# Optimization experiments

Measured on AMD Instinct MI355X. Metric: run time of the kernel, lower is better.

## Reference

```python
import jax, jax.numpy as jnp
import numpy as np

GN_EPS = 1e-5
G = 8          # SKA groups
SKS3 = 27      # sks**3


def _aff(x, s, b):
    # folded BatchNorm (eval): per-channel scale + shift on NCDHW tensor
    return x * s[None, :, None, None, None] + b[None, :, None, None, None]


def _c1(x, w):
    # 1x1x1 conv as channel GEMM; w: [O, I]
    return jnp.einsum('bcdhw,oc->bodhw', x, w)


def _dw5(x, w):
    # depthwise 5x5x5 conv, pad=2; w: [C, 1, 5, 5, 5]
    return jax.lax.conv_general_dilated(
        x, w, window_strides=(1, 1, 1), padding=[(2, 2)] * 3,
        dimension_numbers=('NCDHW', 'OIDHW', 'NCDHW'),
        feature_group_count=x.shape[1])


def setup_inputs() -> dict:
    key = jax.random.key(0)
    ks = jax.random.split(key, 24)
    B, C, D, H, W = 2, 64, 32, 32, 32

    def n(k, shape, scale=1.0):
        return jax.random.normal(k, shape, jnp.float32) * scale

    def u(k, shape):
        return jax.random.uniform(k, shape, jnp.float32, 0.5, 1.5)

    return {
        'x': n(ks[0], (B, C, D, H, W)),
        'w1': n(ks[1], (32, 64), 64 ** -0.5),
        's1': u(ks[2], (32,)), 'b1': n(ks[3], (32,), 0.1),
        'w2': n(ks[4], (32, 1, 5, 5, 5), 125 ** -0.5),
        's2': u(ks[5], (32,)), 'b2': n(ks[6], (32,), 0.1),
        'w3': n(ks[7], (32, 32), 32 ** -0.5),
        's3': u(ks[8], (32,)), 'b3': n(ks[9], (32,), 0.1),
        'w4': n(ks[10], (216, 32), 32 ** -0.5), 'b4': n(ks[11], (216,), 0.1),
        'gn_g': u(ks[12], (216,)), 'gn_b': n(ks[13], (216,), 0.1),
        'bn_s': u(ks[14], (64,)), 'bn_b': n(ks[15], (64,), 0.1),
        'pw1_w': n(ks[16], (128, 64), 64 ** -0.5),
        'pw1_s': u(ks[17], (128,)), 'pw1_b': n(ks[18], (128,), 0.1),
        'pw2_w': n(ks[19], (64, 128), 128 ** -0.5),
        'pw2_s': u(ks[20], (64,)), 'pw2_b': n(ks[21], (64,), 0.1),
    }


def reference(x, w1, s1, b1, w2, s2, b2, w3, s3, b3, w4, b4,
              gn_g, gn_b, bn_s, bn_b,
              pw1_w, pw1_s, pw1_b, pw2_w, pw2_s, pw2_b):
    B, C, D, H, W = x.shape

    # ---- LKP3D: dynamic kernel generation ----
    a = jax.nn.relu(_aff(_c1(x, w1), s1, b1))          # cv1 + BN + ReLU
    a = _aff(_dw5(a, w2), s2, b2)                      # cv2 (5^3 dw) + BN
    a = jax.nn.relu(_aff(_c1(a, w3), s3, b3))          # cv3 + BN + ReLU
    wk = _c1(a, w4) + b4[None, :, None, None, None]    # cv4: [B,216,D,H,W]
    # GroupNorm: num_groups = dim//groups = 8, channels = 216
    g = wk.reshape(B, G, SKS3, D, H, W)
    mu = g.mean(axis=(2, 3, 4, 5), keepdims=True)
    var = g.var(axis=(2, 3, 4, 5), keepdims=True)
    g = (g - mu) * jax.lax.rsqrt(var + GN_EPS)
    wk = g.reshape(B, G * SKS3, D, H, W) * gn_g[None, :, None, None, None] \
         + gn_b[None, :, None, None, None]
    wk = wk.reshape(B, G, SKS3, D, H, W)               # [B, G, 27, D, H, W]

    # ---- SKA3D: apply dynamic kernels (27 shifted copies, grouped) ----
    offs = [(di, hi, wi) for di in (-1, 0, 1) for hi in (-1, 0, 1) for wi in (-1, 0, 1)]
    patches = jnp.stack(
        [jnp.roll(x, (-di, -hi, -wi), axis=(2, 3, 4)) for di, hi, wi in offs],
        axis=2)                                        # [B, C, 27, D, H, W]
    p = patches.reshape(B, G, C // G, SKS3, D, H, W)
    sk = jnp.einsum('bgckdhw,bgkdhw->bgcdhw', p, wk).reshape(B, C, D, H, W)

    y = _aff(sk, bn_s, bn_b) + x                       # LSConv BN + residual

    # ---- FFN (residual): pw1 + BN + ReLU + pw2 + BN ----
    f = jax.nn.relu(_aff(_c1(y, pw1_w), pw1_s, pw1_b))
    f = _aff(_c1(f, pw2_w), pw2_s, pw2_b)
    return y + f
```

## Files before the change

kernel.cpp:

```cpp
#include <hip/hip_runtime.h>
#include <hip/hip_bf16.h>

#define SPAT 32768
#define BATCH 2
#define GN_EPS 1e-5f

__device__ __forceinline__ void fma4(float4& a, const float4& v, float w) {
    a.x = fmaf(v.x, w, a.x); a.y = fmaf(v.y, w, a.y);
    a.z = fmaf(v.z, w, a.z); a.w = fmaf(v.w, w, a.w);
}

template <int OG>
__device__ __forceinline__ void decode_swz(int bid, int& og, int& b, int& s) {
    int xcd = bid & 7;
    int rest = bid >> 3;
    og = rest % OG;
    int pair = rest / OG;
    int spb = pair * 8 + xcd;
    b = spb >> 5;
    s = (spb & 31) * 1024 + threadIdx.x * 4;
}

template <int CIN, int COUT, bool RELU, bool AFF>
__global__ __launch_bounds__(256) void k_pw(
    const float* __restrict__ in, const float* __restrict__ w,
    const float* __restrict__ sc, const float* __restrict__ bi,
    float* __restrict__ out)
{
    constexpr int OG = COUT / 8;
    int og, b, s;
    decode_swz<OG>(blockIdx.x, og, b, s);
    int o0 = og * 8;
    const float* ip = in + (size_t)b * CIN * SPAT + s;
    float4 acc[8];
#pragma unroll
    for (int i = 0; i < 8; ++i) acc[i] = {0, 0, 0, 0};
#pragma unroll 4
    for (int c = 0; c < CIN; ++c) {
        float4 v = *(const float4*)(ip + (size_t)c * SPAT);
#pragma unroll
        for (int i = 0; i < 8; ++i)
            fma4(acc[i], v, w[(o0 + i) * CIN + c]);
    }
#pragma unroll
    for (int i = 0; i < 8; ++i) {
        int o = o0 + i;
        float scale = AFF ? sc[o] : 1.f;
        float shift = bi[o];
        float4 r = acc[i];
        r.x = r.x * scale + shift; r.y = r.y * scale + shift;
        r.z = r.z * scale + shift; r.w = r.w * scale + shift;
        if (RELU) {
            r.x = fmaxf(r.x, 0.f); r.y = fmaxf(r.y, 0.f);
            r.z = fmaxf(r.z, 0.f); r.w = fmaxf(r.w, 0.f);
        }
        *(float4*)(out + ((size_t)b * COUT + o) * SPAT + s) = r;
    }
}

__global__ __launch_bounds__(256) void k_cv4(
    const float* __restrict__ in, const float* __restrict__ w,
    const float* __restrict__ bi, float* __restrict__ out,
    float* __restrict__ partial)
{
    int og, b, s;
    decode_swz<27>(blockIdx.x, og, b, s);
    int sp = s >> 10;
    int o0 = og * 8;
    const float* ip = in + (size_t)b * 32 * SPAT + s;
    float4 acc[8];
#pragma unroll
    for (int i = 0; i < 8; ++i) acc[i] = {0, 0, 0, 0};
#pragma unroll 4
    for (int c = 0; c < 32; ++c) {
        float4 v = *(const float4*)(ip + (size_t)c * SPAT);
#pragma unroll
        for (int i = 0; i < 8; ++i)
            fma4(acc[i], v, w[(o0 + i) * 32 + c]);
    }
    float sums[8], sss[8];
#pragma unroll
    for (int i = 0; i < 8; ++i) {
        int o = o0 + i;
        float shift = bi[o];
        float4 r = acc[i];
        r.x += shift; r.y += shift; r.z += shift; r.w += shift;
        *(float4*)(out + ((size_t)b * 216 + o) * SPAT + s) = r;
        sums[i] = r.x + r.y + r.z + r.w;
        sss[i]  = r.x * r.x + r.y * r.y + r.z * r.z + r.w * r.w;
    }
#pragma unroll
    for (int off = 32; off > 0; off >>= 1) {
#pragma unroll
        for (int i = 0; i < 8; ++i) {
            sums[i] += __shfl_down(sums[i], off, 64);
            sss[i]  += __shfl_down(sss[i],  off, 64);
        }
    }
    __shared__ float sh[4][8][2];
    int wave = threadIdx.x >> 6, lane = threadIdx.x & 63;
    if (lane == 0) {
#pragma unroll
        for (int i = 0; i < 8; ++i) {
            sh[wave][i][0] = sums[i];
            sh[wave][i][1] = sss[i];
        }
    }
    __syncthreads();
    if (threadIdx.x < 8) {
        int i = threadIdx.x;
        float s0 = sh[0][i][0] + sh[1][i][0] + sh[2][i][0] + sh[3][i][0];
        float s1 = sh[0][i][1] + sh[1][i][1] + sh[2][i][1] + sh[3][i][1];
        int o = o0 + i;
        int idx = ((b * 216 + o) * 32 + sp) * 2;
        partial[idx + 0] = s0;
        partial[idx + 1] = s1;
    }
}

__global__ __launch_bounds__(256) void k_gn_stats2(
    const float* __restrict__ partial, float* __restrict__ stats)
{
    int bg = blockIdx.x;
    int b = bg >> 3, g = bg & 7;
    float sum = 0.f, ss = 0.f;
    for (int i = threadIdx.x; i < 27 * 32; i += 256) {
        int o = g * 27 + (i >> 5);
        int xb = i & 31;
        int idx = ((b * 216 + o) * 32 + xb) * 2;
        sum += partial[idx + 0];
        ss  += partial[idx + 1];
    }
    __shared__ float sh[512];
    sh[threadIdx.x] = sum; sh[256 + threadIdx.x] = ss;
    __syncthreads();
    for (int off = 128; off > 0; off >>= 1) {
        if (threadIdx.x < off) {
            sh[threadIdx.x] += sh[threadIdx.x + off];
            sh[256 + threadIdx.x] += sh[256 + threadIdx.x + off];
        }
        __syncthreads();
    }
    if (threadIdx.x == 0) {
        stats[bg * 2 + 0] = sh[0];
        stats[bg * 2 + 1] = sh[256];
    }
}

__global__ __launch_bounds__(256) void k_ska(
    const float* __restrict__ x, const float* __restrict__ wk,
    const float* __restrict__ stats,
    const float* __restrict__ gn_g, const float* __restrict__ gn_b,
    const float* __restrict__ bn_s, const float* __restrict__ bn_b,
    float* __restrict__ y)
{
    int q = blockIdx.x * 256 + threadIdx.x;
    int s = q * 4;
    int g = blockIdx.y, b = blockIdx.z;
    int bg = b * 8 + g;
    const float N = 27.f * (float)SPAT;
    float mu  = stats[bg * 2 + 0] / N;
    float var = stats[bg * 2 + 1] / N - mu * mu;
    float inv = rsqrtf(var + GN_EPS);
    int d = s >> 10, h = (s >> 5) & 31, w0 = s & 31;
    int lane = threadIdx.x & 63;
    int xl_src = (lane & 56) | ((lane + 7) & 7);
    int xr_src = (lane & 56) | ((lane + 1) & 7);
    const float* xg = x + ((size_t)(b * 64 + g * 8)) * SPAT;
    const float* wp = wk + ((size_t)(b * 216 + g * 27)) * SPAT + s;

    float4 acc[8];
    float4 xc[8];
#pragma unroll
    for (int c = 0; c < 8; ++c) acc[c] = {0, 0, 0, 0};

#pragma unroll
    for (int kd = 0; kd < 3; ++kd) {
        int zd = (d + kd + 31) & 31;
#pragma unroll
        for (int kh = 0; kh < 3; ++kh) {
            int zh = (h + kh + 31) & 31;
            int kbase = (kd * 3 + kh) * 3;
            float wn[3][4];
#pragma unroll
            for (int kw = 0; kw < 3; ++kw) {
                int kk = kbase + kw;
                float4 wq = *(const float4*)(wp + (size_t)kk * SPAT);
                float gg = gn_g[g * 27 + kk], gb = gn_b[g * 27 + kk];
                wn[kw][0] = (wq.x - mu) * inv * gg + gb;
                wn[kw][1] = (wq.y - mu) * inv * gg + gb;
                wn[kw][2] = (wq.z - mu) * inv * gg + gb;
                wn[kw][3] = (wq.w - mu) * inv * gg + gb;
            }
            int rowoff = zd * 1024 + zh * 32;
            bool center = (kd == 1) && (kh == 1);
#pragma unroll
            for (int c = 0; c < 8; ++c) {
                float4 m = *(const float4*)(xg + (size_t)c * SPAT + rowoff + w0);
                if (center) xc[c] = m;
                float xl = __shfl(m.w, xl_src, 64);
                float xr = __shfl(m.x, xr_src, 64);
                float win[6] = {xl, m.x, m.y, m.z, m.w, xr};
#pragma unroll
                for (int kw = 0; kw < 3; ++kw) {
                    acc[c].x = fmaf(win[0 + kw], wn[kw][0], acc[c].x);
                    acc[c].y = fmaf(win[1 + kw], wn[kw][1], acc[c].y);
                    acc[c].z = fmaf(win[2 + kw], wn[kw][2], acc[c].z);
                    acc[c].w = fmaf(win[3 + kw], wn[kw][3], acc[c].w);
                }
            }
        }
    }
#pragma unroll
    for (int c = 0; c < 8; ++c) {
        int ch = g * 8 + c;
        float bs = bn_s[ch], bb = bn_b[ch];
        float4 r;
        r.x = acc[c].x * bs + bb + xc[c].x;
        r.y = acc[c].y * bs + bb + xc[c].y;
        r.z = acc[c].z * bs + bb + xc[c].z;
        r.w = acc[c].w * bs + bb + xc[c].w;
        *(float4*)(y + ((size_t)(b * 64 + ch)) * SPAT + s) = r;
    }
}

__global__ __launch_bounds__(256) void k_dw5(
    const float* __restrict__ in, const float* __restrict__ w2,
    const float* __restrict__ s2, const float* __restrict__ b2,
    float* __restrict__ out)
{
    __shared__ float lds[8 * 36 * 40];
    int tid = threadIdx.x;
    int d0 = blockIdx.x * 4;
    int c = blockIdx.y, b = blockIdx.z;
    const float* ip = in + ((size_t)(b * 32 + c)) * SPAT;

    float4 z = {0, 0, 0, 0};
    for (int i = tid; i < 8 * 36 * 40 / 4; i += 256)
        ((float4*)lds)[i] = z;
    __syncthreads();
    for (int i = tid; i < 8 * 256; i += 256) {
        int p = i >> 8, rem = i & 255;
        int r = rem >> 3, c4 = (rem & 7) * 4;
        int d = d0 - 2 + p;
        if (d >= 0 && d < 32) {
            float4 v = *(const float4*)(ip + d * 1024 + r * 32 + c4);
            *(float4*)&lds[p * 1440 + (r + 2) * 40 + (c4 + 4)] = v;
        }
    }
    __syncthreads();

    float scl = s2[c], shf = b2[c];
    const float* wt = w2 + c * 125;
#pragma unroll
    for (int k = 0; k < 4; ++k) {
        int j = tid + k * 256;
        int pd = j >> 8, rem = j & 255;
        int hr = rem >> 3, w4 = (rem & 7) * 4;
        float4 acc = {0, 0, 0, 0};
#pragma unroll
        for (int kd = 0; kd < 5; ++kd) {
            const float* pl = &lds[(pd + kd) * 1440];
#pragma unroll
            for (int kh = 0; kh < 5; ++kh) {
                const float* row = pl + (hr + kh) * 40 + w4;
                float4 r0 = *(const float4*)(row);
                float4 r1 = *(const float4*)(row + 4);
                float4 r2 = *(const float4*)(row + 8);
                float win[12] = {r0.x, r0.y, r0.z, r0.w,
                                 r1.x, r1.y, r1.z, r1.w,
                                 r2.x, r2.y, r2.z, r2.w};
#pragma unroll
                for (int kw = 0; kw < 5; ++kw) {
                    float wv = wt[kd * 25 + kh * 5 + kw];
                    acc.x = fmaf(wv, win[2 + 0 + kw], acc.x);
                    acc.y = fmaf(wv, win[2 + 1 + kw], acc.y);
                    acc.z = fmaf(wv, win[2 + 2 + kw], acc.z);
                    acc.w = fmaf(wv, win[2 + 3 + kw], acc.w);
                }
            }
        }
        acc.x = acc.x * scl + shf; acc.y = acc.y * scl + shf;
        acc.z = acc.z * scl + shf; acc.w = acc.w * scl + shf;
        *(float4*)(out + ((size_t)(b * 32 + c)) * SPAT
                   + (d0 + pd) * 1024 + hr * 32 + w4) = acc;
    }
}

__global__ __launch_bounds__(256) void k_pw2_out(
    const float* __restrict__ f1, const float* __restrict__ w,
    const float* __restrict__ sc, const float* __restrict__ bi,
    const float* __restrict__ yres, float* __restrict__ out)
{
    int og, b, s;
    decode_swz<8>(blockIdx.x, og, b, s);
    int o0 = og * 8;
    const float* ip = f1 + (size_t)b * 128 * SPAT + s;
    float4 acc[8];
#pragma unroll
    for (int i = 0; i < 8; ++i) acc[i] = {0, 0, 0, 0};
#pragma unroll 4
    for (int c = 0; c < 128; ++c) {
        float4 v = *(const float4*)(ip + (size_t)c * SPAT);
#pragma unroll
        for (int i = 0; i < 8; ++i)
            fma4(acc[i], v, w[(o0 + i) * 128 + c]);
    }
#pragma unroll
    for (int i = 0; i < 8; ++i) {
        int o = o0 + i;
        float scale = sc[o], shift = bi[o];
        float4 yv = *(const float4*)(yres + ((size_t)(b * 64 + o)) * SPAT + s);
        float4 r = acc[i];
        r.x = r.x * scale + shift + yv.x;
        r.y = r.y * scale + shift + yv.y;
        r.z = r.z * scale + shift + yv.z;
        r.w = r.w * scale + shift + yv.w;
        *(float4*)(out + ((size_t)(b * 64 + o)) * SPAT + s) = r;
    }
}

extern "C" void kernel_launch(void* const* d_in, const int* in_sizes, int n_in,
                              void* d_out, int out_size, void* d_ws, size_t ws_size,
                              hipStream_t stream)
{
    const float* x     = (const float*)d_in[0];
    const float* w1    = (const float*)d_in[1];
    const float* s1    = (const float*)d_in[2];
    const float* b1    = (const float*)d_in[3];
    const float* w2    = (const float*)d_in[4];
    const float* s2    = (const float*)d_in[5];
    const float* b2    = (const float*)d_in[6];
    const float* w3    = (const float*)d_in[7];
    const float* s3    = (const float*)d_in[8];
    const float* b3    = (const float*)d_in[9];
    const float* w4    = (const float*)d_in[10];
    const float* b4    = (const float*)d_in[11];
    const float* gn_g  = (const float*)d_in[12];
    const float* gn_b  = (const float*)d_in[13];
    const float* bn_s  = (const float*)d_in[14];
    const float* bn_b  = (const float*)d_in[15];
    const float* pw1_w = (const float*)d_in[16];
    const float* pw1_s = (const float*)d_in[17];
    const float* pw1_b = (const float*)d_in[18];
    const float* pw2_w = (const float*)d_in[19];
    const float* pw2_s = (const float*)d_in[20];
    const float* pw2_b = (const float*)d_in[21];

    float* ws    = (float*)d_ws;
    float* a1    = ws;
    float* a2    = a1 + (size_t)BATCH * 32 * SPAT;
    float* yb    = ws;
    float* wkb   = ws + (size_t)BATCH * 64 * SPAT;
    float* f1    = wkb;
    float* part  = wkb + (size_t)BATCH * 216 * SPAT;
    float* stats = part + BATCH * 216 * 32 * 2;

    dim3 blk(256);
    k_pw<64, 32, true, true><<<dim3(4 * 64), blk, 0, stream>>>(x, w1, s1, b1, a1);
    k_dw5<<<dim3(8, 32, BATCH), blk, 0, stream>>>(a1, w2, s2, b2, a2);
    k_pw<32, 32, true, true><<<dim3(4 * 64), blk, 0, stream>>>(a2, w3, s3, b3, a1);
    k_cv4<<<dim3(27 * 64), blk, 0, stream>>>(a1, w4, b4, wkb, part);
    k_gn_stats2<<<dim3(16), blk, 0, stream>>>(part, stats);
    k_ska<<<dim3(SPAT / 1024, 8, BATCH), blk, 0, stream>>>(
        x, wkb, stats, gn_g, gn_b, bn_s, bn_b, yb);
    k_pw<64, 128, true, true><<<dim3(16 * 64), blk, 0, stream>>>(
        yb, pw1_w, pw1_s, pw1_b, f1);
    k_pw2_out<<<dim3(8 * 64), blk, 0, stream>>>(
        f1, pw2_w, pw2_s, pw2_b, yb, (float*)d_out);
}
```

Baseline: 234.3 us.

## Fuse SKA aggregation with both FFN pointwise convs through LDS

Merges the dynamic-kernel aggregation, residual, FFN expand and FFN project into one kernel per 256-voxel tile. The intermediate y is staged in a swizzled LDS buffer and the 128-channel hidden activation stays in registers, so those tensors no longer round-trip through global memory. The first two pointwise convs move to a simpler kernel with runtime channel counts and 4 outputs per block. The fused kernel uses very large per-thread register arrays and 64KB of LDS, which risks spills, low occupancy and a small grid.

```diff
diff --git a/kernel.cpp b/kernel.cpp
--- a/kernel.cpp
+++ b/kernel.cpp
@@ -8,6 +8,42 @@
 __device__ __forceinline__ void fma4(float4& a, const float4& v, float w) {
     a.x = fmaf(v.x, w, a.x); a.y = fmaf(v.y, w, a.y);
     a.z = fmaf(v.z, w, a.z); a.w = fmaf(v.w, w, a.w);
+}
+
+template <bool RELU, bool AFF>
+__global__ __launch_bounds__(256) void k_c1(
+    const float* __restrict__ in, const float* __restrict__ w,
+    const float* __restrict__ sc, const float* __restrict__ bi,
+    float* __restrict__ out, int Cin, int Cout)
+{
+    int q = blockIdx.x * 256 + threadIdx.x;
+    int s = q * 4;
+    int o0 = blockIdx.y * 4, b = blockIdx.z;
+    const float* ip = in + (size_t)b * Cin * SPAT + s;
+    float4 a0 = {0,0,0,0}, a1 = a0, a2 = a0, a3 = a0;
+#pragma unroll 4
+    for (int c = 0; c < Cin; ++c) {
+        float4 v = *(const float4*)(ip + (size_t)c * SPAT);
+        fma4(a0, v, w[(o0+0)*Cin + c]);
+        fma4(a1, v, w[(o0+1)*Cin + c]);
+        fma4(a2, v, w[(o0+2)*Cin + c]);
+        fma4(a3, v, w[(o0+3)*Cin + c]);
+    }
+    float4 accs[4] = {a0, a1, a2, a3};
+#pragma unroll
+    for (int i = 0; i < 4; ++i) {
+        int o = o0 + i;
+        float scale = AFF ? sc[o] : 1.f;
+        float shift = bi[o];
+        float4 r = accs[i];
+        r.x = r.x * scale + shift; r.y = r.y * scale + shift;
+        r.z = r.z * scale + shift; r.w = r.w * scale + shift;
+        if (RELU) {
+            r.x = fmaxf(r.x, 0.f); r.y = fmaxf(r.y, 0.f);
+            r.z = fmaxf(r.z, 0.f); r.w = fmaxf(r.w, 0.f);
+        }
+        *(float4*)(out + ((size_t)b * Cout + o) * SPAT + s) = r;
+    }
 }
 
 template <int OG>
@@ -21,43 +57,6 @@
     s = (spb & 31) * 1024 + threadIdx.x * 4;
 }
 
-template <int CIN, int COUT, bool RELU, bool AFF>
-__global__ __launch_bounds__(256) void k_pw(
-    const float* __restrict__ in, const float* __restrict__ w,
-    const float* __restrict__ sc, const float* __restrict__ bi,
-    float* __restrict__ out)
-{
-    constexpr int OG = COUT / 8;
-    int og, b, s;
-    decode_swz<OG>(blockIdx.x, og, b, s);
-    int o0 = og * 8;
-    const float* ip = in + (size_t)b * CIN * SPAT + s;
-    float4 acc[8];
-#pragma unroll
-    for (int i = 0; i < 8; ++i) acc[i] = {0, 0, 0, 0};
-#pragma unroll 4
-    for (int c = 0; c < CIN; ++c) {
-        float4 v = *(const float4*)(ip + (size_t)c * SPAT);
-#pragma unroll
-        for (int i = 0; i < 8; ++i)
-            fma4(acc[i], v, w[(o0 + i) * CIN + c]);
-    }
-#pragma unroll
-    for (int i = 0; i < 8; ++i) {
-        int o = o0 + i;
-        float scale = AFF ? sc[o] : 1.f;
-        float shift = bi[o];
-        float4 r = acc[i];
-        r.x = r.x * scale + shift; r.y = r.y * scale + shift;
-        r.z = r.z * scale + shift; r.w = r.w * scale + shift;
-        if (RELU) {
-            r.x = fmaxf(r.x, 0.f); r.y = fmaxf(r.y, 0.f);
-            r.z = fmaxf(r.z, 0.f); r.w = fmaxf(r.w, 0.f);
-        }
-        *(float4*)(out + ((size_t)b * COUT + o) * SPAT + s) = r;
-    }
-}
-
 __global__ __launch_bounds__(256) void k_cv4(
     const float* __restrict__ in, const float* __restrict__ w,
     const float* __restrict__ bi, float* __restrict__ out,
@@ -147,83 +146,6 @@
     }
 }
 
-__global__ __launch_bounds__(256) void k_ska(
-    const float* __restrict__ x, const float* __restrict__ wk,
-    const float* __restrict__ stats,
-    const float* __restrict__ gn_g, const float* __restrict__ gn_b,
-    const float* __restrict__ bn_s, const float* __restrict__ bn_b,
-    float* __restrict__ y)
-{
-    int q = blockIdx.x * 256 + threadIdx.x;
-    int s = q * 4;
-    int g = blockIdx.y, b = blockIdx.z;
-    int bg = b * 8 + g;
-    const float N = 27.f * (float)SPAT;
-    float mu  = stats[bg * 2 + 0] / N;
-    float var = stats[bg * 2 + 1] / N - mu * mu;
-    float inv = rsqrtf(var + GN_EPS);
-    int d = s >> 10, h = (s >> 5) & 31, w0 = s & 31;
-    int lane = threadIdx.x & 63;
-    int xl_src = (lane & 56) | ((lane + 7) & 7);
-    int xr_src = (lane & 56) | ((lane + 1) & 7);
-    const float* xg = x + ((size_t)(b * 64 + g * 8)) * SPAT;
-    const float* wp = wk + ((size_t)(b * 216 + g * 27)) * SPAT + s;
-
-    float4 acc[8];
-    float4 xc[8];
-#pragma unroll
-    for (int c = 0; c < 8; ++c) acc[c] = {0, 0, 0, 0};
-
-#pragma unroll
-    for (int kd = 0; kd < 3; ++kd) {
-        int zd = (d + kd + 31) & 31;
-#pragma unroll
-        for (int kh = 0; kh < 3; ++kh) {
-            int zh = (h + kh + 31) & 31;
-            int kbase = (kd * 3 + kh) * 3;
-            float wn[3][4];
-#pragma unroll
-            for (int kw = 0; kw < 3; ++kw) {
-                int kk = kbase + kw;
-                float4 wq = *(const float4*)(wp + (size_t)kk * SPAT);
-                float gg = gn_g[g * 27 + kk], gb = gn_b[g * 27 + kk];
-                wn[kw][0] = (wq.x - mu) * inv * gg + gb;
-                wn[kw][1] = (wq.y - mu) * inv * gg + gb;
-                wn[kw][2] = (wq.z - mu) * inv * gg + gb;
-                wn[kw][3] = (wq.w - mu) * inv * gg + gb;
-            }
-            int rowoff = zd * 1024 + zh * 32;
-            bool center = (kd == 1) && (kh == 1);
-#pragma unroll
-            for (int c = 0; c < 8; ++c) {
-                float4 m = *(const float4*)(xg + (size_t)c * SPAT + rowoff + w0);
-                if (center) xc[c] = m;
-                float xl = __shfl(m.w, xl_src, 64);
-                float xr = __shfl(m.x, xr_src, 64);
-                float win[6] = {xl, m.x, m.y, m.z, m.w, xr};
-#pragma unroll
-                for (int kw = 0; kw < 3; ++kw) {
-                    acc[c].x = fmaf(win[0 + kw], wn[kw][0], acc[c].x);
-                    acc[c].y = fmaf(win[1 + kw], wn[kw][1], acc[c].y);
-                    acc[c].z = fmaf(win[2 + kw], wn[kw][2], acc[c].z);
-                    acc[c].w = fmaf(win[3 + kw], wn[kw][3], acc[c].w);
-                }
-            }
-        }
-    }
-#pragma unroll
-    for (int c = 0; c < 8; ++c) {
-        int ch = g * 8 + c;
-        float bs = bn_s[ch], bb = bn_b[ch];
-        float4 r;
-        r.x = acc[c].x * bs + bb + xc[c].x;
-        r.y = acc[c].y * bs + bb + xc[c].y;
-        r.z = acc[c].z * bs + bb + xc[c].z;
-        r.w = acc[c].w * bs + bb + xc[c].w;
-        *(float4*)(y + ((size_t)(b * 64 + ch)) * SPAT + s) = r;
-    }
-}
-
 __global__ __launch_bounds__(256) void k_dw5(
     const float* __restrict__ in, const float* __restrict__ w2,
     const float* __restrict__ s2, const float* __restrict__ b2,
@@ -287,36 +209,141 @@
     }
 }
 
-__global__ __launch_bounds__(256) void k_pw2_out(
-    const float* __restrict__ f1, const float* __restrict__ w,
-    const float* __restrict__ sc, const float* __restrict__ bi,
-    const float* __restrict__ yres, float* __restrict__ out)
-{
-    int og, b, s;
-    decode_swz<8>(blockIdx.x, og, b, s);
-    int o0 = og * 8;
-    const float* ip = f1 + (size_t)b * 128 * SPAT + s;
-    float4 acc[8];
-#pragma unroll
-    for (int i = 0; i < 8; ++i) acc[i] = {0, 0, 0, 0};
-#pragma unroll 4
-    for (int c = 0; c < 128; ++c) {
-        float4 v = *(const float4*)(ip + (size_t)c * SPAT);
-#pragma unroll
-        for (int i = 0; i < 8; ++i)
-            fma4(acc[i], v, w[(o0 + i) * 128 + c]);
-    }
-#pragma unroll
-    for (int i = 0; i < 8; ++i) {
-        int o = o0 + i;
-        float scale = sc[o], shift = bi[o];
-        float4 yv = *(const float4*)(yres + ((size_t)(b * 64 + o)) * SPAT + s);
-        float4 r = acc[i];
-        r.x = r.x * scale + shift + yv.x;
-        r.y = r.y * scale + shift + yv.y;
-        r.z = r.z * scale + shift + yv.z;
-        r.w = r.w * scale + shift + yv.w;
-        *(float4*)(out + ((size_t)(b * 64 + o)) * SPAT + s) = r;
+__global__ __launch_bounds__(256) void k_ska_ffn(
+    const float* __restrict__ x, const float* __restrict__ wk,
+    const float* __restrict__ stats,
+    const float* __restrict__ gn_g, const float* __restrict__ gn_b,
+    const float* __restrict__ bn_s, const float* __restrict__ bn_b,
+    const float* __restrict__ w1, const float* __restrict__ s1f,
+    const float* __restrict__ b1f,
+    const float* __restrict__ w2, const float* __restrict__ s2f,
+    const float* __restrict__ b2f,
+    float* __restrict__ out)
+{
+    __shared__ float yl[256 * 64];
+    int tid = threadIdx.x;
+    int cid = blockIdx.x;
+    int b = cid >> 7;
+    int s0 = (cid & 127) * 256;
+    int d0 = s0 >> 10;
+    int h0 = (s0 >> 5) & 31;
+
+    int g = tid >> 5, u = tid & 31;
+    int lane = tid & 63;
+    int xl_src = (lane & 56) | ((lane + 7) & 7);
+    int xr_src = (lane & 56) | ((lane + 1) & 7);
+    int bg = b * 8 + g;
+    const float N = 27.f * (float)SPAT;
+    float mu  = stats[bg * 2 + 0] / N;
+    float var = stats[bg * 2 + 1] / N - mu * mu;
+    float inv = rsqrtf(var + GN_EPS);
+    const float* xg  = x + ((size_t)(b * 64 + g * 8)) * SPAT;
+    const float* wpb = wk + ((size_t)(b * 216 + g * 27)) * SPAT;
+
+#pragma unroll
+    for (int pass = 0; pass < 2; ++pass) {
+        int q = u + pass * 32;
+        int h = h0 + (q >> 3);
+        int w0 = (q & 7) * 4;
+        int sq = s0 + q * 4;
+        const float* wp = wpb + sq;
+
+        float4 acc[8];
+        float4 xc[8];
+#pragma unroll
+        for (int c = 0; c < 8; ++c) acc[c] = {0, 0, 0, 0};
+
+#pragma unroll
+        for (int kd = 0; kd < 3; ++kd) {
+            int zd = (d0 + kd + 31) & 31;
+#pragma unroll
+            for (int kh = 0; kh < 3; ++kh) {
+                int zh = (h + kh + 31) & 31;
+                int kbase = (kd * 3 + kh) * 3;
+                float wn[3][4];
+#pragma unroll
+                for (int kw = 0; kw < 3; ++kw) {
+                    int kk = kbase + kw;
+                    float4 wq = *(const float4*)(wp + (size_t)kk * SPAT);
+                    float gg = gn_g[g * 27 + kk], gb = gn_b[g * 27 + kk];
+                    wn[kw][0] = (wq.x - mu) * inv * gg + gb;
+                    wn[kw][1] = (wq.y - mu) * inv * gg + gb;
+                    wn[kw][2] = (wq.z - mu) * inv * gg + gb;
+                    wn[kw][3] = (wq.w - mu) * inv * gg + gb;
+                }
+                int rowoff = zd * 1024 + zh * 32;
+                bool center = (kd == 1) && (kh == 1);
+#pragma unroll
+                for (int c = 0; c < 8; ++c) {
+                    float4 m = *(const float4*)(xg + (size_t)c * SPAT + rowoff + w0);
+                    if (center) xc[c] = m;
+                    float xl = __shfl(m.w, xl_src, 64);
+                    float xr = __shfl(m.x, xr_src, 64);
+                    float win[6] = {xl, m.x, m.y, m.z, m.w, xr};
+#pragma unroll
+                    for (int kw = 0; kw < 3; ++kw) {
+                        acc[c].x = fmaf(win[0 + kw], wn[kw][0], acc[c].x);
+                        acc[c].y = fmaf(win[1 + kw], wn[kw][1], acc[c].y);
+                        acc[c].z = fmaf(win[2 + kw], wn[kw][2], acc[c].z);
+                        acc[c].w = fmaf(win[3 + kw], wn[kw][3], acc[c].w);
+                    }
+                }
+            }
+        }
+#pragma unroll
+        for (int c = 0; c < 8; ++c) {
+            int ch = g * 8 + c;
+            float bs = bn_s[ch], bb = bn_b[ch];
+            float4 r;
+            r.x = acc[c].x * bs + bb + xc[c].x;
+            r.y = acc[c].y * bs + bb + xc[c].y;
+            r.z = acc[c].z * bs + bb + xc[c].z;
+            r.w = acc[c].w * bs + bb + xc[c].w;
+            int p0 = q * 4;
+            yl[(p0 + 0) * 64 + ((ch + p0 + 0) & 63)] = r.x;
+            yl[(p0 + 1) * 64 + ((ch + p0 + 1) & 63)] = r.y;
+            yl[(p0 + 2) * 64 + ((ch + p0 + 2) & 63)] = r.z;
+            yl[(p0 + 3) * 64 + ((ch + p0 + 3) & 63)] = r.w;
+        }
+    }
+    __syncthreads();
+
+    int p = tid;
+    float yv[64];
+#pragma unroll
+    for (int c = 0; c < 64; ++c) yv[c] = yl[p * 64 + ((c + p) & 63)];
+
+    float outacc[64];
+#pragma unroll
+    for (int o = 0; o < 64; ++o) outacc[o] = 0.f;
+
+    for (int t = 0; t < 8; ++t) {
+        int j0 = t * 16;
+        float f[16];
+#pragma unroll
+        for (int jj = 0; jj < 16; ++jj) {
+            int j = j0 + jj;
+            const float* wr = w1 + j * 64;
+            float a = 0.f;
+#pragma unroll
+            for (int c = 0; c < 64; ++c) a = fmaf(wr[c], yv[c], a);
+            a = a * s1f[j] + b1f[j];
+            f[jj] = fmaxf(a, 0.f);
+        }
+#pragma unroll
+        for (int o = 0; o < 64; ++o) {
+            const float* w2r = w2 + o * 128 + j0;
+            float a = outacc[o];
+#pragma unroll
+            for (int jj = 0; jj < 16; ++jj) a = fmaf(w2r[jj], f[jj], a);
+            outacc[o] = a;
+        }
+    }
+    float* op = out + (size_t)b * 64 * SPAT + s0 + p;
+#pragma unroll
+    for (int o = 0; o < 64; ++o) {
+        float r = outacc[o] * s2f[o] + b2f[o] + yl[p * 64 + ((o + p) & 63)];
+        op[(size_t)o * SPAT] = r;
     }
 }
 
@@ -350,22 +377,19 @@
     float* ws    = (float*)d_ws;
     float* a1    = ws;
     float* a2    = a1 + (size_t)BATCH * 32 * SPAT;
-    float* yb    = ws;
-    float* wkb   = ws + (size_t)BATCH * 64 * SPAT;
-    float* f1    = wkb;
+    float* wkb   = a2 + (size_t)BATCH * 32 * SPAT;
     float* part  = wkb + (size_t)BATCH * 216 * SPAT;
     float* stats = part + BATCH * 216 * 32 * 2;
 
     dim3 blk(256);
-    k_pw<64, 32, true, true><<<dim3(4 * 64), blk, 0, stream>>>(x, w1, s1, b1, a1);
+    k_c1<true, true><<<dim3(SPAT / 1024, 8, BATCH), blk, 0, stream>>>(
+        x, w1, s1, b1, a1, 64, 32);
     k_dw5<<<dim3(8, 32, BATCH), blk, 0, stream>>>(a1, w2, s2, b2, a2);
-    k_pw<32, 32, true, true><<<dim3(4 * 64), blk, 0, stream>>>(a2, w3, s3, b3, a1);
+    k_c1<true, true><<<dim3(SPAT / 1024, 8, BATCH), blk, 0, stream>>>(
+        a2, w3, s3, b3, a1, 32, 32);
     k_cv4<<<dim3(27 * 64), blk, 0, stream>>>(a1, w4, b4, wkb, part);
     k_gn_stats2<<<dim3(16), blk, 0, stream>>>(part, stats);
-    k_ska<<<dim3(SPAT / 1024, 8, BATCH), blk, 0, stream>>>(
-        x, wkb, stats, gn_g, gn_b, bn_s, bn_b, yb);
-    k_pw<64, 128, true, true><<<dim3(16 * 64), blk, 0, stream>>>(
-        yb, pw1_w, pw1_s, pw1_b, f1);
-    k_pw2_out<<<dim3(8 * 64), blk, 0, stream>>>(
-        f1, pw2_w, pw2_s, pw2_b, yb, (float*)d_out);
-}
+    k_ska_ffn<<<dim3(BATCH * (SPAT / 256)), blk, 0, stream>>>(
+        x, wkb, stats, gn_g, gn_b, bn_s, bn_b,
+        pw1_w, pw1_s, pw1_b, pw2_w, pw2_s, pw2_b, (float*)d_out);
+}
```

Measured after the change: 400.8 us. +71.1%, slower.

## Replace scalar pointwise convs with bf16 MFMA GEMM kernel

Applied to the files above, without the earlier changes.

All five 1x1x1 channel GEMMs (cv1, cv3, cv4 with GN partial stats, pw1, pw2 with residual) now use one templated kernel. It stages a 128-position tile and the weights in LDS as bf16 and computes with 16x16x32 bf16 MFMA instructions, replacing per-thread fp32 FMA loops. cv4 output is padded to 224 channels, and GN partials are collected per wave, so the stats kernel now reduces 1024 chunks per channel. Workspace buffers are laid out separately instead of aliasing. The bf16 inputs lower precision, and the LDS transpose stores are scalar 2-byte writes that may bank-conflict.

```diff
diff --git a/kernel.cpp b/kernel.cpp
--- a/kernel.cpp
+++ b/kernel.cpp
@@ -4,117 +4,112 @@
 #define SPAT 32768
 #define BATCH 2
 #define GN_EPS 1e-5f
-
-__device__ __forceinline__ void fma4(float4& a, const float4& v, float w) {
-    a.x = fmaf(v.x, w, a.x); a.y = fmaf(v.y, w, a.y);
-    a.z = fmaf(v.z, w, a.z); a.w = fmaf(v.w, w, a.w);
-}
-
-template <int OG>
-__device__ __forceinline__ void decode_swz(int bid, int& og, int& b, int& s) {
-    int xcd = bid & 7;
-    int rest = bid >> 3;
-    og = rest % OG;
-    int pair = rest / OG;
-    int spb = pair * 8 + xcd;
-    b = spb >> 5;
-    s = (spb & 31) * 1024 + threadIdx.x * 4;
-}
-
-template <int CIN, int COUT, bool RELU, bool AFF>
-__global__ __launch_bounds__(256) void k_pw(
+#define CPAD 224
+
+typedef __attribute__((ext_vector_type(8))) short bf16x8;
+typedef __attribute__((ext_vector_type(4))) float f32x4;
+
+__device__ __forceinline__ short f2bf(float f) {
+    __hip_bfloat16 h = __float2bfloat16(f);
+    return *reinterpret_cast<short*>(&h);
+}
+
+template <int CIN, int COUT, int COUT_REAL, bool RELU, bool AFF, bool STATS, bool RES>
+__global__ __launch_bounds__(256) void k_mfma_pw(
     const float* __restrict__ in, const float* __restrict__ w,
     const float* __restrict__ sc, const float* __restrict__ bi,
-    float* __restrict__ out)
-{
-    constexpr int OG = COUT / 8;
-    int og, b, s;
-    decode_swz<OG>(blockIdx.x, og, b, s);
-    int o0 = og * 8;
-    const float* ip = in + (size_t)b * CIN * SPAT + s;
-    float4 acc[8];
-#pragma unroll
-    for (int i = 0; i < 8; ++i) acc[i] = {0, 0, 0, 0};
-#pragma unroll 4
-    for (int c = 0; c < CIN; ++c) {
-        float4 v = *(const float4*)(ip + (size_t)c * SPAT);
-#pragma unroll
-        for (int i = 0; i < 8; ++i)
-            fma4(acc[i], v, w[(o0 + i) * CIN + c]);
-    }
-#pragma unroll
-    for (int i = 0; i < 8; ++i) {
-        int o = o0 + i;
+    const float* __restrict__ yres,
+    float* __restrict__ out, float* __restrict__ partial)
+{
+    constexpr int LT = CIN + 8;
+    constexpr int KS = CIN / 32;
+    constexpr int NT = COUT / 16;
+    __shared__ short lt[128 * LT];
+    __shared__ short wt[COUT * LT];
+    int tid = threadIdx.x;
+    int b = blockIdx.z;
+    int s0 = blockIdx.x * 128;
+
+    const float* ip = in + (size_t)b * CIN * SPAT + s0;
+#pragma unroll
+    for (int it = 0; it < CIN / 8; ++it) {
+        int j = tid + it * 256;
+        int c = j >> 5;
+        int p4 = (j & 31) * 4;
+        float4 v = *(const float4*)(ip + (size_t)c * SPAT + p4);
+        lt[(p4 + 0) * LT + c] = f2bf(v.x);
+        lt[(p4 + 1) * LT + c] = f2bf(v.y);
+        lt[(p4 + 2) * LT + c] = f2bf(v.z);
+        lt[(p4 + 3) * LT + c] = f2bf(v.w);
+    }
+#pragma unroll
+    for (int it = 0; it < COUT * CIN / 256; ++it) {
+        int j = tid + it * 256;
+        int o = j / CIN, c = j % CIN;
+        float wv = (COUT == COUT_REAL || o < COUT_REAL) ? w[o * CIN + c] : 0.f;
+        wt[o * LT + c] = f2bf(wv);
+    }
+    __syncthreads();
+
+    int wave = tid >> 6, lane = tid & 63, quad = lane >> 4, l15 = lane & 15;
+    int wp0 = wave * 32;
+
+    bf16x8 afr[2][KS];
+#pragma unroll
+    for (int m = 0; m < 2; ++m) {
+        int p = wp0 + m * 16 + l15;
+#pragma unroll
+        for (int kk = 0; kk < KS; ++kk)
+            afr[m][kk] = *(const bf16x8*)&lt[p * LT + kk * 32 + quad * 8];
+    }
+
+    for (int nt = 0; nt < NT; ++nt) {
+        int o = nt * 16 + l15;
+        bf16x8 bfr[KS];
+#pragma unroll
+        for (int kk = 0; kk < KS; ++kk)
+            bfr[kk] = *(const bf16x8*)&wt[o * LT + kk * 32 + quad * 8];
+        f32x4 acc[2] = {{0.f, 0.f, 0.f, 0.f}, {0.f, 0.f, 0.f, 0.f}};
+#pragma unroll
+        for (int kk = 0; kk < KS; ++kk) {
+            acc[0] = __builtin_amdgcn_mfma_f32_16x16x32_bf16(afr[0][kk], bfr[kk], acc[0], 0, 0, 0);
+            acc[1] = __builtin_amdgcn_mfma_f32_16x16x32_bf16(afr[1][kk], bfr[kk], acc[1], 0, 0, 0);
+        }
         float scale = AFF ? sc[o] : 1.f;
-        float shift = bi[o];
-        float4 r = acc[i];
-        r.x = r.x * scale + shift; r.y = r.y * scale + shift;
-        r.z = r.z * scale + shift; r.w = r.w * scale + shift;
-        if (RELU) {
-            r.x = fmaxf(r.x, 0.f); r.y = fmaxf(r.y, 0.f);
-            r.z = fmaxf(r.z, 0.f); r.w = fmaxf(r.w, 0.f);
-        }
-        *(float4*)(out + ((size_t)b * COUT + o) * SPAT + s) = r;
-    }
-}
-
-__global__ __launch_bounds__(256) void k_cv4(
-    const float* __restrict__ in, const float* __restrict__ w,
-    const float* __restrict__ bi, float* __restrict__ out,
-    float* __restrict__ partial)
-{
-    int og, b, s;
-    decode_swz<27>(blockIdx.x, og, b, s);
-    int sp = s >> 10;
-    int o0 = og * 8;
-    const float* ip = in + (size_t)b * 32 * SPAT + s;
-    float4 acc[8];
-#pragma unroll
-    for (int i = 0; i < 8; ++i) acc[i] = {0, 0, 0, 0};
-#pragma unroll 4
-    for (int c = 0; c < 32; ++c) {
-        float4 v = *(const float4*)(ip + (size_t)c * SPAT);
-#pragma unroll
-        for (int i = 0; i < 8; ++i)
-            fma4(acc[i], v, w[(o0 + i) * 32 + c]);
-    }
-    float sums[8], sss[8];
-#pragma unroll
-    for (int i = 0; i < 8; ++i) {
-        int o = o0 + i;
-        float shift = bi[o];
-        float4 r = acc[i];
-        r.x += shift; r.y += shift; r.z += shift; r.w += shift;
-        *(float4*)(out + ((size_t)b * 216 + o) * SPAT + s) = r;
-        sums[i] = r.x + r.y + r.z + r.w;
-        sss[i]  = r.x * r.x + r.y * r.y + r.z * r.z + r.w * r.w;
-    }
-#pragma unroll
-    for (int off = 32; off > 0; off >>= 1) {
-#pragma unroll
-        for (int i = 0; i < 8; ++i) {
-            sums[i] += __shfl_down(sums[i], off, 64);
-            sss[i]  += __shfl_down(sss[i],  off, 64);
-        }
-    }
-    __shared__ float sh[4][8][2];
-    int wave = threadIdx.x >> 6, lane = threadIdx.x & 63;
-    if (lane == 0) {
-#pragma unroll
-        for (int i = 0; i < 8; ++i) {
-            sh[wave][i][0] = sums[i];
-            sh[wave][i][1] = sss[i];
-        }
-    }
-    __syncthreads();
-    if (threadIdx.x < 8) {
-        int i = threadIdx.x;
-        float s0 = sh[0][i][0] + sh[1][i][0] + sh[2][i][0] + sh[3][i][0];
-        float s1 = sh[0][i][1] + sh[1][i][1] + sh[2][i][1] + sh[3][i][1];
-        int o = o0 + i;
-        int idx = ((b * 216 + o) * 32 + sp) * 2;
-        partial[idx + 0] = s0;
-        partial[idx + 1] = s1;
+        float shift = (COUT == COUT_REAL || o < COUT_REAL) ? bi[o] : 0.f;
+        float psum = 0.f, pss = 0.f;
+#pragma unroll
+        for (int m = 0; m < 2; ++m) {
+            int pos = s0 + wp0 + m * 16 + quad * 4;
+            float4 r;
+            r.x = acc[m][0] * scale + shift;
+            r.y = acc[m][1] * scale + shift;
+            r.z = acc[m][2] * scale + shift;
+            r.w = acc[m][3] * scale + shift;
+            if (RELU) {
+                r.x = fmaxf(r.x, 0.f); r.y = fmaxf(r.y, 0.f);
+                r.z = fmaxf(r.z, 0.f); r.w = fmaxf(r.w, 0.f);
+            }
+            if (RES) {
+                float4 yv = *(const float4*)(yres + ((size_t)(b * COUT + o)) * SPAT + pos);
+                r.x += yv.x; r.y += yv.y; r.z += yv.z; r.w += yv.w;
+            }
+            *(float4*)(out + ((size_t)b * COUT + o) * SPAT + pos) = r;
+            if (STATS) {
+                psum += r.x + r.y + r.z + r.w;
+                pss  += r.x * r.x + r.y * r.y + r.z * r.z + r.w * r.w;
+            }
+        }
+        if (STATS) {
+            psum += __shfl_xor(psum, 16, 64); pss += __shfl_xor(pss, 16, 64);
+            psum += __shfl_xor(psum, 32, 64); pss += __shfl_xor(pss, 32, 64);
+            if (quad == 0) {
+                int chunk = blockIdx.x * 4 + wave;
+                int idx = (((b * COUT + o) << 10) + chunk) * 2;
+                partial[idx + 0] = psum;
+                partial[idx + 1] = pss;
+            }
+        }
     }
 }
 
@@ -124,10 +119,10 @@
     int bg = blockIdx.x;
     int b = bg >> 3, g = bg & 7;
     float sum = 0.f, ss = 0.f;
-    for (int i = threadIdx.x; i < 27 * 32; i += 256) {
-        int o = g * 27 + (i >> 5);
-        int xb = i & 31;
-        int idx = ((b * 216 + o) * 32 + xb) * 2;
+    for (int i = threadIdx.x; i < 27 * 1024; i += 256) {
+        int o = g * 27 + (i >> 10);
+        int ch = i & 1023;
+        int idx = (((b * CPAD + o) << 10) + ch) * 2;
         sum += partial[idx + 0];
         ss  += partial[idx + 1];
     }
@@ -144,6 +139,69 @@
     if (threadIdx.x == 0) {
         stats[bg * 2 + 0] = sh[0];
         stats[bg * 2 + 1] = sh[256];
+    }
+}
+
+__global__ __launch_bounds__(256) void k_dw5(
+    const float* __restrict__ in, const float* __restrict__ w2,
+    const float* __restrict__ s2, const float* __restrict__ b2,
+    float* __restrict__ out)
+{
+    __shared__ float lds[8 * 36 * 40];
+    int tid = threadIdx.x;
+    int d0 = blockIdx.x * 4;
+    int c = blockIdx.y, b = blockIdx.z;
+    const float* ip = in + ((size_t)(b * 32 + c)) * SPAT;
+
+    float4 z = {0, 0, 0, 0};
+    for (int i = tid; i < 8 * 36 * 40 / 4; i += 256)
+        ((float4*)lds)[i] = z;
+    __syncthreads();
+    for (int i = tid; i < 8 * 256; i += 256) {
+        int p = i >> 8, rem = i & 255;
+        int r = rem >> 3, c4 = (rem & 7) * 4;
+        int d = d0 - 2 + p;
+        if (d >= 0 && d < 32) {
+            float4 v = *(const float4*)(ip + d * 1024 + r * 32 + c4);
+            *(float4*)&lds[p * 1440 + (r + 2) * 40 + (c4 + 4)] = v;
+        }
+    }
+    __syncthreads();
+
+    float scl = s2[c], shf = b2[c];
+    const float* wt = w2 + c * 125;
+#pragma unroll
+    for (int k = 0; k < 4; ++k) {
+        int j = tid + k * 256;
+        int pd = j >> 8, rem = j & 255;
+        int hr = rem >> 3, w4 = (rem & 7) * 4;
+        float4 acc = {0, 0, 0, 0};
+#pragma unroll
+        for (int kd = 0; kd < 5; ++kd) {
+            const float* pl = &lds[(pd + kd) * 1440];
+#pragma unroll
+            for (int kh = 0; kh < 5; ++kh) {
+                const float* row = pl + (hr + kh) * 40 + w4;
+                float4 r0 = *(const float4*)(row);
+                float4 r1 = *(const float4*)(row + 4);
+                float4 r2 = *(const float4*)(row + 8);
+                float win[12] = {r0.x, r0.y, r0.z, r0.w,
+                                 r1.x, r1.y, r1.z, r1.w,
+                                 r2.x, r2.y, r2.z, r2.w};
+#pragma unroll
+                for (int kw = 0; kw < 5; ++kw) {
+                    float wv = wt[kd * 25 + kh * 5 + kw];
+                    acc.x = fmaf(wv, win[2 + 0 + kw], acc.x);
+                    acc.y = fmaf(wv, win[2 + 1 + kw], acc.y);
+                    acc.z = fmaf(wv, win[2 + 2 + kw], acc.z);
+                    acc.w = fmaf(wv, win[2 + 3 + kw], acc.w);
+                }
+            }
+        }
+        acc.x = acc.x * scl + shf; acc.y = acc.y * scl + shf;
+        acc.z = acc.z * scl + shf; acc.w = acc.w * scl + shf;
+        *(float4*)(out + ((size_t)(b * 32 + c)) * SPAT
+                   + (d0 + pd) * 1024 + hr * 32 + w4) = acc;
     }
 }
 
@@ -167,7 +225,7 @@
     int xl_src = (lane & 56) | ((lane + 7) & 7);
     int xr_src = (lane & 56) | ((lane + 1) & 7);
     const float* xg = x + ((size_t)(b * 64 + g * 8)) * SPAT;
-    const float* wp = wk + ((size_t)(b * 216 + g * 27)) * SPAT + s;
+    const float* wp = wk + ((size_t)(b * CPAD + g * 27)) * SPAT + s;
 
     float4 acc[8];
     float4 xc[8];
@@ -221,102 +279,6 @@
         r.z = acc[c].z * bs + bb + xc[c].z;
         r.w = acc[c].w * bs + bb + xc[c].w;
         *(float4*)(y + ((size_t)(b * 64 + ch)) * SPAT + s) = r;
-    }
-}
-
-__global__ __launch_bounds__(256) void k_dw5(
-    const float* __restrict__ in, const float* __restrict__ w2,
-    const float* __restrict__ s2, const float* __restrict__ b2,
-    float* __restrict__ out)
-{
-    __shared__ float lds[8 * 36 * 40];
-    int tid = threadIdx.x;
-    int d0 = blockIdx.x * 4;
-    int c = blockIdx.y, b = blockIdx.z;
-    const float* ip = in + ((size_t)(b * 32 + c)) * SPAT;
-
-    float4 z = {0, 0, 0, 0};
-    for (int i = tid; i < 8 * 36 * 40 / 4; i += 256)
-        ((float4*)lds)[i] = z;
-    __syncthreads();
-    for (int i = tid; i < 8 * 256; i += 256) {
-        int p = i >> 8, rem = i & 255;
-        int r = rem >> 3, c4 = (rem & 7) * 4;
-        int d = d0 - 2 + p;
-        if (d >= 0 && d < 32) {
-            float4 v = *(const float4*)(ip + d * 1024 + r * 32 + c4);
-            *(float4*)&lds[p * 1440 + (r + 2) * 40 + (c4 + 4)] = v;
-        }
-    }
-    __syncthreads();
-
-    float scl = s2[c], shf = b2[c];
-    const float* wt = w2 + c * 125;
-#pragma unroll
-    for (int k = 0; k < 4; ++k) {
-        int j = tid + k * 256;
-        int pd = j >> 8, rem = j & 255;
-        int hr = rem >> 3, w4 = (rem & 7) * 4;
-        float4 acc = {0, 0, 0, 0};
-#pragma unroll
-        for (int kd = 0; kd < 5; ++kd) {
-            const float* pl = &lds[(pd + kd) * 1440];
-#pragma unroll
-            for (int kh = 0; kh < 5; ++kh) {
-                const float* row = pl + (hr + kh) * 40 + w4;
-                float4 r0 = *(const float4*)(row);
-                float4 r1 = *(const float4*)(row + 4);
-                float4 r2 = *(const float4*)(row + 8);
-                float win[12] = {r0.x, r0.y, r0.z, r0.w,
-                                 r1.x, r1.y, r1.z, r1.w,
-                                 r2.x, r2.y, r2.z, r2.w};
-#pragma unroll
-                for (int kw = 0; kw < 5; ++kw) {
-                    float wv = wt[kd * 25 + kh * 5 + kw];
-                    acc.x = fmaf(wv, win[2 + 0 + kw], acc.x);
-                    acc.y = fmaf(wv, win[2 + 1 + kw], acc.y);
-                    acc.z = fmaf(wv, win[2 + 2 + kw], acc.z);
-                    acc.w = fmaf(wv, win[2 + 3 + kw], acc.w);
-                }
-            }
-        }
-        acc.x = acc.x * scl + shf; acc.y = acc.y * scl + shf;
-        acc.z = acc.z * scl + shf; acc.w = acc.w * scl + shf;
-        *(float4*)(out + ((size_t)(b * 32 + c)) * SPAT
-                   + (d0 + pd) * 1024 + hr * 32 + w4) = acc;
-    }
-}
-
-__global__ __launch_bounds__(256) void k_pw2_out(
-    const float* __restrict__ f1, const float* __restrict__ w,
-    const float* __restrict__ sc, const float* __restrict__ bi,
-    const float* __restrict__ yres, float* __restrict__ out)
-{
-    int og, b, s;
-    decode_swz<8>(blockIdx.x, og, b, s);
-    int o0 = og * 8;
-    const float* ip = f1 + (size_t)b * 128 * SPAT + s;
-    float4 acc[8];
-#pragma unroll
-    for (int i = 0; i < 8; ++i) acc[i] = {0, 0, 0, 0};
-#pragma unroll 4
-    for (int c = 0; c < 128; ++c) {
-        float4 v = *(const float4*)(ip + (size_t)c * SPAT);
-#pragma unroll
-        for (int i = 0; i < 8; ++i)
-            fma4(acc[i], v, w[(o0 + i) * 128 + c]);
-    }
-#pragma unroll
-    for (int i = 0; i < 8; ++i) {
-        int o = o0 + i;
-        float scale = sc[o], shift = bi[o];
-        float4 yv = *(const float4*)(yres + ((size_t)(b * 64 + o)) * SPAT + s);
-        float4 r = acc[i];
-        r.x = r.x * scale + shift + yv.x;
-        r.y = r.y * scale + shift + yv.y;
-        r.z = r.z * scale + shift + yv.z;
-        r.w = r.w * scale + shift + yv.w;
-        *(float4*)(out + ((size_t)(b * 64 + o)) * SPAT + s) = r;
     }
 }
 
@@ -350,22 +312,26 @@
     float* ws    = (float*)d_ws;
     float* a1    = ws;
     float* a2    = a1 + (size_t)BATCH * 32 * SPAT;
-    float* yb    = ws;
-    float* wkb   = ws + (size_t)BATCH * 64 * SPAT;
-    float* f1    = wkb;
-    float* part  = wkb + (size_t)BATCH * 216 * SPAT;
-    float* stats = part + BATCH * 216 * 32 * 2;
+    float* yb    = a2 + (size_t)BATCH * 32 * SPAT;
+    float* wkb   = yb + (size_t)BATCH * 64 * SPAT;
+    float* f1    = wkb + (size_t)BATCH * CPAD * SPAT;
+    float* part  = f1 + (size_t)BATCH * 128 * SPAT;
+    float* stats = part + (size_t)BATCH * CPAD * 1024 * 2;
 
     dim3 blk(256);
-    k_pw<64, 32, true, true><<<dim3(4 * 64), blk, 0, stream>>>(x, w1, s1, b1, a1);
+    dim3 gmm(SPAT / 128, 1, BATCH);
+    k_mfma_pw<64, 32, 32, true, true, false, false><<<gmm, blk, 0, stream>>>(
+        x, w1, s1, b1, nullptr, a1, nullptr);
     k_dw5<<<dim3(8, 32, BATCH), blk, 0, stream>>>(a1, w2, s2, b2, a2);
-    k_pw<32, 32, true, true><<<dim3(4 * 64), blk, 0, stream>>>(a2, w3, s3, b3, a1);
-    k_cv4<<<dim3(27 * 64), blk, 0, stream>>>(a1, w4, b4, wkb, part);
+    k_mfma_pw<32, 32, 32, true, true, false, false><<<gmm, blk, 0, stream>>>(
+        a2, w3, s3, b3, nullptr, a1, nullptr);
+    k_mfma_pw<32, CPAD, 216, false, false, true, false><<<gmm, blk, 0, stream>>>(
+        a1, w4, nullptr, b4, nullptr, wkb, part);
     k_gn_stats2<<<dim3(16), blk, 0, stream>>>(part, stats);
     k_ska<<<dim3(SPAT / 1024, 8, BATCH), blk, 0, stream>>>(
         x, wkb, stats, gn_g, gn_b, bn_s, bn_b, yb);
-    k_pw<64, 128, true, true><<<dim3(16 * 64), blk, 0, stream>>>(
-        yb, pw1_w, pw1_s, pw1_b, f1);
-    k_pw2_out<<<dim3(8 * 64), blk, 0, stream>>>(
-        f1, pw2_w, pw2_s, pw2_b, yb, (float*)d_out);
-}
+    k_mfma_pw<64, 128, 128, true, true, false, false><<<gmm, blk, 0, stream>>>(
+        yb, pw1_w, pw1_s, pw1_b, nullptr, f1, nullptr);
+    k_mfma_pw<128, 64, 64, false, true, false, true><<<gmm, blk, 0, stream>>>(
+        f1, pw2_w, pw2_s, pw2_b, yb, (float*)d_out, nullptr);
+}
```

Result: no change. 232.7 us (-0.6%).
